# Performance work log

Measured on AMD Instinct MI355X. Metric: run time of the kernel, lower is better.

The kernel has to match this reference:

```python
import jax, jax.numpy as jnp
import numpy as np

N_ATOMS = 500_000
N_PAIRS = 16_000_000
A0 = 0.5291772105638411
KE = 14.399645351950548
KEHALF = KE / 2.0


def softplus_inverse(x):
    # inverse of softplus: log(exp(x) - 1)
    return float(np.log(np.expm1(x)))


def setup_inputs() -> dict:
    key = jax.random.key(0)
    k_z, k_r, k_c, k_i, k_j = jax.random.split(key, 5)
    Zf = jax.random.randint(k_z, (N_ATOMS,), 1, 95).astype(jnp.float32)
    rij = jax.random.uniform(k_r, (N_PAIRS,), minval=0.5, maxval=5.0, dtype=jnp.float32)
    cutoff_values = jax.random.uniform(k_c, (N_PAIRS,), dtype=jnp.float32)
    idx_i = jax.random.randint(k_i, (N_PAIRS,), 0, N_ATOMS)
    idx_j = jax.random.randint(k_j, (N_PAIRS,), 0, N_ATOMS)
    p = lambda v: jnp.full((1,), softplus_inverse(v), dtype=jnp.float32)
    return {
        "N": N_ATOMS,
        "Zf": Zf,
        "rij": rij,
        "cutoff_values": cutoff_values,
        "idx_i": idx_i,
        "idx_j": idx_j,
        "adiv": p(1.0 / (0.8854 * A0)),
        "apow": p(0.23),
        "c1": p(0.1818),
        "c2": p(0.5099),
        "c3": p(0.2802),
        "c4": p(0.02817),
        "a1": p(3.2),
        "a2": p(0.9423),
        "a3": p(0.4028),
        "a4": p(0.2016),
    }


def reference(N, Zf, rij, cutoff_values, idx_i, idx_j,
              adiv, apow, c1, c2, c3, c4, a1, a2, a3, a4):
    sp = jax.nn.softplus
    # per-atom screened charge: [N]
    z = Zf ** sp(apow)
    # per-pair screening length: [P]
    a = (z[idx_i] + z[idx_j]) * sp(adiv)
    a1p = sp(a1) * a
    a2p = sp(a2) * a
    a3p = sp(a3) * a
    a4p = sp(a4) * a
    c1p, c2p, c3p, c4p = sp(c1), sp(c2), sp(c3), sp(c4)
    csum = c1p + c2p + c3p + c4p
    c1n, c2n, c3n, c4n = c1p / csum, c2p / csum, c3p / csum, c4p / csum
    zizj = Zf[idx_i] * Zf[idx_j]
    f = (c1n * jnp.exp(-a1p * rij)
         + c2n * jnp.exp(-a2p * rij)
         + c3n * jnp.exp(-a3p * rij)
         + c4n * jnp.exp(-a4p * rij)) * cutoff_values
    contrib = KEHALF * f * zizj / rij  # [P]
    return jnp.zeros((N,), dtype=Zf.dtype).at[idx_i].add(contrib)
```

## Files before the change

### kernel.cpp

```cpp
#include <hip/hip_runtime.h>
#include <hip/hip_fp16.h>

static constexpr float KEHALF = 7.199822675975274f;
static constexpr int APB = 2048;
static constexpr int APB_SHIFT = 11;
static constexpr int NBMAX = 256;
static constexpr int CHUNK = 8192;
static constexpr int ABLK = 512;
static constexpr int BBLK = 1024;
static constexpr int CTILE = 1024;
static constexpr int NW_SCAN = NBMAX / 64;

typedef float v4f __attribute__((ext_vector_type(4)));
typedef int   v4i __attribute__((ext_vector_type(4)));
typedef unsigned v4u __attribute__((ext_vector_type(4)));

__global__ void zbl_tables_kernel(const float* __restrict__ adiv,
                                  const float* __restrict__ apow,
                                  const float* __restrict__ c1,
                                  const float* __restrict__ c2,
                                  const float* __restrict__ c3,
                                  const float* __restrict__ c4,
                                  const float* __restrict__ a1,
                                  const float* __restrict__ a2,
                                  const float* __restrict__ a3,
                                  const float* __restrict__ a4,
                                  float* __restrict__ consts) {
    if (threadIdx.x == 0) {
        auto sp = [](float x) { return log1pf(expf(x)); };
        float c1p = sp(*c1), c2p = sp(*c2), c3p = sp(*c3), c4p = sp(*c4);
        float inv = 1.0f / (c1p + c2p + c3p + c4p);
        consts[0] = sp(*apow);
        consts[1] = sp(*adiv);
        consts[2] = c1p * inv; consts[3] = c2p * inv;
        consts[4] = c3p * inv; consts[5] = c4p * inv;
        consts[6] = sp(*a1); consts[7] = sp(*a2);
        consts[8] = sp(*a3); consts[9] = sp(*a4);
    }
}

__global__ void zbl_pack_kernel(const float* __restrict__ Zf,
                                unsigned char* __restrict__ zb, int N) {
    int i = blockIdx.x * blockDim.x + threadIdx.x;
    if (i < N) zb[i] = (unsigned char)(Zf[i] + 0.5f);
}

__global__ void __launch_bounds__(ABLK)
zbl_phaseA(const int* __restrict__ idx_i, const int* __restrict__ idx_j,
           const float* __restrict__ rij, const float* __restrict__ cut,
           const unsigned char* __restrict__ zb,
           const float* __restrict__ consts,
           unsigned* __restrict__ recs, unsigned short* __restrict__ starts,
           int P, int NB, int nchunks) {
    __shared__ unsigned hist[NBMAX];
    __shared__ unsigned cursor[NBMAX];
    __shared__ unsigned wsum[NW_SCAN];
    __shared__ unsigned stage[CHUNK];

    const int t = threadIdx.x;
    const int c = blockIdx.x;
    const int base = c * CHUNK;
    const int cnt = min(base + CHUNK, P) - base;
    const int n4 = cnt >> 2;

    for (int b = t; b < NBMAX; b += ABLK) hist[b] = 0;
    __syncthreads();

    const v4i* ii4 = reinterpret_cast<const v4i*>(idx_i + base);
    const bool p0 = t < n4;
    const bool p1 = ABLK + t < n4;
    const bool p2 = 2 * ABLK + t < n4;
    const bool p3 = 3 * ABLK + t < n4;
    v4i ii0{}, ii1{}, ii2{}, ii3{};
    if (p0) ii0 = __builtin_nontemporal_load(ii4 + t);
    if (p1) ii1 = __builtin_nontemporal_load(ii4 + ABLK + t);
    if (p2) ii2 = __builtin_nontemporal_load(ii4 + 2 * ABLK + t);
    if (p3) ii3 = __builtin_nontemporal_load(ii4 + 3 * ABLK + t);

    auto packb = [&](v4i ii) -> unsigned {
        return (unsigned)zb[ii[0]] | ((unsigned)zb[ii[1]] << 8)
             | ((unsigned)zb[ii[2]] << 16) | ((unsigned)zb[ii[3]] << 24);
    };
    unsigned bp0 = 0, bp1 = 0, bp2 = 0, bp3 = 0;
    if (p0) bp0 = packb(ii0);
    if (p1) bp1 = packb(ii1);
    if (p2) bp2 = packb(ii2);
    if (p3) bp3 = packb(ii3);

    auto hist4 = [&](v4i ii) {
        atomicAdd(&hist[(unsigned)ii[0] >> APB_SHIFT], 1u);
        atomicAdd(&hist[(unsigned)ii[1] >> APB_SHIFT], 1u);
        atomicAdd(&hist[(unsigned)ii[2] >> APB_SHIFT], 1u);
        atomicAdd(&hist[(unsigned)ii[3] >> APB_SHIFT], 1u);
    };
    if (p0) hist4(ii0);
    if (p1) hist4(ii1);
    if (p2) hist4(ii2);
    if (p3) hist4(ii3);
    for (int p = n4 * 4 + t; p < cnt; p += ABLK)
        atomicAdd(&hist[(unsigned)idx_i[base + p] >> APB_SHIFT], 1u);
    __syncthreads();

    unsigned hv = (t < NBMAX) ? hist[t] : 0u;
    unsigned v = hv;
#pragma unroll
    for (int off = 1; off < 64; off <<= 1) {
        unsigned n = __shfl_up(v, off, 64);
        if ((t & 63) >= off) v += n;
    }
    if (t < NBMAX && (t & 63) == 63) wsum[t >> 6] = v;
    __syncthreads();
    if (t < NBMAX) {
        unsigned pre = 0;
#pragma unroll
        for (int w = 0; w < NW_SCAN - 1; ++w)
            if (w < (t >> 6)) pre += wsum[w];
        unsigned inc = v + pre;
        cursor[t] = inc - hv;
        if (t < NB)
            starts[(size_t)(t + 1) * nchunks + c] = (unsigned short)inc;
    }
    if (t == 0) starts[c] = 0;
    __syncthreads();

    const float sp_apow = consts[0], sp_adiv = consts[1];
    const float c1n = consts[2], c2n = consts[3], c3n = consts[4], c4n = consts[5];
    const float a1 = consts[6], a2 = consts[7], a3 = consts[8], a4 = consts[9];

    auto process = [&](int i, unsigned bi, unsigned bj, float r, float cu) {
        float fi = (float)bi, fj = (float)bj;
        float zi = __expf(sp_apow * __logf(fi));
        float zj = __expf(sp_apow * __logf(fj));
        float ar = (zi + zj) * sp_adiv * r;
        float f = c1n * __expf(-a1 * ar) + c2n * __expf(-a2 * ar)
                + c3n * __expf(-a3 * ar) + c4n * __expf(-a4 * ar);
        float contrib = KEHALF * f * cu * fi * fj * __builtin_amdgcn_rcpf(r);
        unsigned b = (unsigned)i >> APB_SHIFT;
        unsigned rank = atomicAdd(&cursor[b], 1u);
        stage[rank] = (((unsigned)i & (APB - 1)) << 16)
                    | (unsigned)__half_as_ushort(__float2half_rn(contrib));
    };

    const v4i* jj4 = reinterpret_cast<const v4i*>(idx_j + base);
    const v4f* rr4 = reinterpret_cast<const v4f*>(rij + base);
    const v4f* cc4 = reinterpret_cast<const v4f*>(cut + base);
    auto group = [&](v4i ii, unsigned bp, int q) {
        v4i jj = __builtin_nontemporal_load(jj4 + q);
        v4f rr = __builtin_nontemporal_load(rr4 + q);
        v4f cc = __builtin_nontemporal_load(cc4 + q);
#pragma unroll
        for (int k = 0; k < 4; ++k)
            process(ii[k], (bp >> (8 * k)) & 0xffu, zb[jj[k]], rr[k], cc[k]);
    };
    if (p0) group(ii0, bp0, t);
    if (p1) group(ii1, bp1, ABLK + t);
    if (p2) group(ii2, bp2, 2 * ABLK + t);
    if (p3) group(ii3, bp3, 3 * ABLK + t);
    for (int p = n4 * 4 + t; p < cnt; p += ABLK) {
        int i = idx_i[base + p];
        process(i, zb[i], zb[idx_j[base + p]], rij[base + p], cut[base + p]);
    }
    __syncthreads();

    {
        const v4u* src = reinterpret_cast<const v4u*>(stage);
        v4u* dst = reinterpret_cast<v4u*>(recs + (size_t)base);
        for (int k = t; k < CHUNK / 4; k += ABLK)
            __builtin_nontemporal_store(src[k], dst + k);
    }
}

__global__ void __launch_bounds__(BBLK)
zbl_phaseB(const unsigned* __restrict__ recs,
           const unsigned short* __restrict__ starts,
           float* __restrict__ out, int N, int NB, int nchunks, int cpb) {
    __shared__ float acc[APB];
    __shared__ unsigned short s0s[CTILE];
    __shared__ unsigned short s1s[CTILE];
    const int t = threadIdx.x;
    const int b = blockIdx.x;
    const int c0 = blockIdx.y * cpb;
    const int c1e = min(c0 + cpb, nchunks);
    for (int i = t; i < APB; i += BBLK) acc[i] = 0.f;

    const unsigned short* s0row = starts + (size_t)b * nchunks;
    const unsigned short* s1row = starts + (size_t)(b + 1) * nchunks;
    const int hw = t >> 5, hl = t & 31, nhw = BBLK / 32;

    for (int cb = c0; cb < c1e; cb += CTILE) {
        const int ce = min(cb + CTILE, c1e);
        __syncthreads();
        for (int c = cb + t; c < ce; c += BBLK) {
            s0s[c - cb] = s0row[c];
            s1s[c - cb] = s1row[c];
        }
        __syncthreads();
        for (int c = cb + hw; c < ce; c += nhw) {
            unsigned s0 = s0s[c - cb], s1 = s1s[c - cb];
            const unsigned* seg = recs + (size_t)c * CHUNK;
            for (unsigned u = s0 + hl; u < s1; u += 32) {
                unsigned rec = __builtin_nontemporal_load(seg + u);
                float v = __half2float(__ushort_as_half((unsigned short)(rec & 0xffffu)));
                atomicAdd(&acc[rec >> 16], v);
            }
        }
    }
    __syncthreads();
    const int abase = b << APB_SHIFT;
    for (int i = t; i < APB; i += BBLK) {
        int g = abase + i;
        if (g < N) atomicAdd(&out[g], acc[i]);
    }
}

__global__ void __launch_bounds__(256)
zbl_pair_fallback(const v4f* __restrict__ rij4, const v4f* __restrict__ cut4,
                  const v4i* __restrict__ ii4, const v4i* __restrict__ jj4,
                  const float* __restrict__ Zf, const float* __restrict__ consts,
                  float* __restrict__ out, int P4) {
    int t = blockIdx.x * blockDim.x + threadIdx.x;
    if (t >= P4) return;
    const float sp_apow = consts[0], sp_adiv = consts[1];
    const float c1n = consts[2], c2n = consts[3], c3n = consts[4], c4n = consts[5];
    const float a1 = consts[6], a2 = consts[7], a3 = consts[8], a4 = consts[9];
    v4f rr = rij4[t]; v4f cc = cut4[t]; v4i ii = ii4[t]; v4i jj = jj4[t];
#pragma unroll
    for (int k = 0; k < 4; ++k) {
        int i = ii[k], j = jj[k];
        float zfi = Zf[i], zfj = Zf[j];
        float zi = __expf(sp_apow * __logf(zfi));
        float zj = __expf(sp_apow * __logf(zfj));
        float a = (zi + zj) * sp_adiv;
        float ar = a * rr[k];
        float f = c1n * __expf(-a1 * ar) + c2n * __expf(-a2 * ar)
                + c3n * __expf(-a3 * ar) + c4n * __expf(-a4 * ar);
        atomicAdd(&out[i],
                  KEHALF * f * cc[k] * zfi * zfj * __builtin_amdgcn_rcpf(rr[k]));
    }
}

extern "C" void kernel_launch(void* const* d_in, const int* in_sizes, int n_in,
                              void* d_out, int out_size, void* d_ws, size_t ws_size,
                              hipStream_t stream) {
    const float* Zf = (const float*)d_in[1];
    const float* rij = (const float*)d_in[2];
    const float* cut = (const float*)d_in[3];
    const int* idx_i = (const int*)d_in[4];
    const int* idx_j = (const int*)d_in[5];
    const int N = in_sizes[1];
    const int P = in_sizes[2];
    float* out = (float*)d_out;

    const int NB = (N + APB - 1) / APB;
    const int nchunks = (P + CHUNK - 1) / CHUNK;

    size_t recs_bytes = (size_t)nchunks * CHUNK * 4;
    size_t starts_bytes = (size_t)(NB + 1) * nchunks * 2;
    size_t consts_off = (recs_bytes + starts_bytes + 255) & ~(size_t)255;
    size_t zb_off = consts_off + 16 * 4;
    size_t need = zb_off + (size_t)N + 64;

    if (NB <= NBMAX && ws_size >= need) {
        unsigned* recs = (unsigned*)d_ws;
        unsigned short* starts = (unsigned short*)((char*)d_ws + recs_bytes);
        float* consts = (float*)((char*)d_ws + consts_off);
        unsigned char* zb = (unsigned char*)((char*)d_ws + zb_off);

        zbl_tables_kernel<<<1, 64, 0, stream>>>(
            (const float*)d_in[6], (const float*)d_in[7],
            (const float*)d_in[8], (const float*)d_in[9],
            (const float*)d_in[10], (const float*)d_in[11],
            (const float*)d_in[12], (const float*)d_in[13],
            (const float*)d_in[14], (const float*)d_in[15], consts);

        zbl_pack_kernel<<<(N + 255) / 256, 256, 0, stream>>>(Zf, zb, N);

        hipMemsetAsync(out, 0, (size_t)out_size * sizeof(float), stream);

        zbl_phaseA<<<nchunks, ABLK, 0, stream>>>(
            idx_i, idx_j, rij, cut, zb, consts, recs, starts, P, NB, nchunks);

        int SPLIT = (2048 + NB - 1) / NB;
        if (SPLIT < 1) SPLIT = 1;
        if (SPLIT > 16) SPLIT = 16;
        const int cpb = (nchunks + SPLIT - 1) / SPLIT;
        dim3 gridB(NB, SPLIT);
        zbl_phaseB<<<gridB, BBLK, 0, stream>>>(recs, starts, out, N, NB,
                                               nchunks, cpb);
    } else {
        float* consts = (float*)d_ws;
        hipMemsetAsync(out, 0, (size_t)out_size * sizeof(float), stream);
        zbl_tables_kernel<<<1, 64, 0, stream>>>(
            (const float*)d_in[6], (const float*)d_in[7],
            (const float*)d_in[8], (const float*)d_in[9],
            (const float*)d_in[10], (const float*)d_in[11],
            (const float*)d_in[12], (const float*)d_in[13],
            (const float*)d_in[14], (const float*)d_in[15], consts);
        zbl_pair_fallback<<<(P / 4 + 255) / 256, 256, 0, stream>>>(
            (const v4f*)rij, (const v4f*)cut, (const v4i*)idx_i,
            (const v4i*)idx_j, Zf, consts, out, P / 4);
    }
}
```

Before: 453.7 us.

## Fuse prep kernels, tabulate per-Z screening, prefetch j-charges, drop nontemporal hints

Merges the constants, Z-packing and output-zeroing launches into one prep kernel, which removes two launches and a memset. Phase A now builds a 96-entry shared table of softplus(adiv)*Z^softplus(apow), replacing the per-pair log/exp pow with a table lookup. It also loads idx_j early so both charge gathers are issued together. Nontemporal load/store hints are replaced with plain accesses, and the phase-B split factor is raised to give more blocks. The plain accesses may change cache behaviour for the streamed data, and the table assumes Z values below 96.

```diff
diff --git a/kernel.cpp b/kernel.cpp
--- a/kernel.cpp
+++ b/kernel.cpp
@@ -14,6 +14,22 @@
 typedef float v4f __attribute__((ext_vector_type(4)));
 typedef int   v4i __attribute__((ext_vector_type(4)));
 typedef unsigned v4u __attribute__((ext_vector_type(4)));
+
+__device__ __forceinline__ void compute_consts(
+        const float* adiv, const float* apow,
+        const float* c1, const float* c2, const float* c3, const float* c4,
+        const float* a1, const float* a2, const float* a3, const float* a4,
+        float* consts) {
+    auto sp = [](float x) { return log1pf(expf(x)); };
+    float c1p = sp(*c1), c2p = sp(*c2), c3p = sp(*c3), c4p = sp(*c4);
+    float inv = 1.0f / (c1p + c2p + c3p + c4p);
+    consts[0] = sp(*apow);
+    consts[1] = sp(*adiv);
+    consts[2] = c1p * inv; consts[3] = c2p * inv;
+    consts[4] = c3p * inv; consts[5] = c4p * inv;
+    consts[6] = sp(*a1); consts[7] = sp(*a2);
+    consts[8] = sp(*a3); consts[9] = sp(*a4);
+}
 
 __global__ void zbl_tables_kernel(const float* __restrict__ adiv,
                                   const float* __restrict__ apow,
@@ -26,23 +42,31 @@
                                   const float* __restrict__ a3,
                                   const float* __restrict__ a4,
                                   float* __restrict__ consts) {
-    if (threadIdx.x == 0) {
-        auto sp = [](float x) { return log1pf(expf(x)); };
-        float c1p = sp(*c1), c2p = sp(*c2), c3p = sp(*c3), c4p = sp(*c4);
-        float inv = 1.0f / (c1p + c2p + c3p + c4p);
-        consts[0] = sp(*apow);
-        consts[1] = sp(*adiv);
-        consts[2] = c1p * inv; consts[3] = c2p * inv;
-        consts[4] = c3p * inv; consts[5] = c4p * inv;
-        consts[6] = sp(*a1); consts[7] = sp(*a2);
-        consts[8] = sp(*a3); consts[9] = sp(*a4);
-    }
-}
-
-__global__ void zbl_pack_kernel(const float* __restrict__ Zf,
-                                unsigned char* __restrict__ zb, int N) {
+    if (threadIdx.x == 0)
+        compute_consts(adiv, apow, c1, c2, c3, c4, a1, a2, a3, a4, consts);
+}
+
+__global__ void zbl_prep(const float* __restrict__ Zf,
+                         unsigned char* __restrict__ zb,
+                         float* __restrict__ out, int N,
+                         const float* __restrict__ adiv,
+                         const float* __restrict__ apow,
+                         const float* __restrict__ c1,
+                         const float* __restrict__ c2,
+                         const float* __restrict__ c3,
+                         const float* __restrict__ c4,
+                         const float* __restrict__ a1,
+                         const float* __restrict__ a2,
+                         const float* __restrict__ a3,
+                         const float* __restrict__ a4,
+                         float* __restrict__ consts) {
     int i = blockIdx.x * blockDim.x + threadIdx.x;
-    if (i < N) zb[i] = (unsigned char)(Zf[i] + 0.5f);
+    if (i < N) {
+        zb[i] = (unsigned char)(Zf[i] + 0.5f);
+        out[i] = 0.0f;
+    }
+    if (blockIdx.x == 0 && threadIdx.x == 0)
+        compute_consts(adiv, apow, c1, c2, c3, c4, a1, a2, a3, a4, consts);
 }
 
 __global__ void __launch_bounds__(ABLK)
@@ -55,6 +79,7 @@
     __shared__ unsigned hist[NBMAX];
     __shared__ unsigned cursor[NBMAX];
     __shared__ unsigned wsum[NW_SCAN];
+    __shared__ float lA[96];
     __shared__ unsigned stage[CHUNK];
 
     const int t = threadIdx.x;
@@ -64,28 +89,33 @@
     const int n4 = cnt >> 2;
 
     for (int b = t; b < NBMAX; b += ABLK) hist[b] = 0;
+    if (t < 96)
+        lA[t] = (t == 0) ? 0.0f
+                         : consts[1] * __expf(consts[0] * __logf((float)t));
     __syncthreads();
 
     const v4i* ii4 = reinterpret_cast<const v4i*>(idx_i + base);
+    const v4i* jj4 = reinterpret_cast<const v4i*>(idx_j + base);
     const bool p0 = t < n4;
     const bool p1 = ABLK + t < n4;
     const bool p2 = 2 * ABLK + t < n4;
     const bool p3 = 3 * ABLK + t < n4;
-    v4i ii0{}, ii1{}, ii2{}, ii3{};
-    if (p0) ii0 = __builtin_nontemporal_load(ii4 + t);
-    if (p1) ii1 = __builtin_nontemporal_load(ii4 + ABLK + t);
-    if (p2) ii2 = __builtin_nontemporal_load(ii4 + 2 * ABLK + t);
-    if (p3) ii3 = __builtin_nontemporal_load(ii4 + 3 * ABLK + t);
-
-    auto packb = [&](v4i ii) -> unsigned {
-        return (unsigned)zb[ii[0]] | ((unsigned)zb[ii[1]] << 8)
-             | ((unsigned)zb[ii[2]] << 16) | ((unsigned)zb[ii[3]] << 24);
+    v4i ii0{}, ii1{}, ii2{}, ii3{}, jj0{}, jj1{}, jj2{}, jj3{};
+    if (p0) { ii0 = ii4[t];            jj0 = jj4[t]; }
+    if (p1) { ii1 = ii4[ABLK + t];     jj1 = jj4[ABLK + t]; }
+    if (p2) { ii2 = ii4[2 * ABLK + t]; jj2 = jj4[2 * ABLK + t]; }
+    if (p3) { ii3 = ii4[3 * ABLK + t]; jj3 = jj4[3 * ABLK + t]; }
+
+    auto packb = [&](v4i ix) -> unsigned {
+        return (unsigned)zb[ix[0]] | ((unsigned)zb[ix[1]] << 8)
+             | ((unsigned)zb[ix[2]] << 16) | ((unsigned)zb[ix[3]] << 24);
     };
-    unsigned bp0 = 0, bp1 = 0, bp2 = 0, bp3 = 0;
-    if (p0) bp0 = packb(ii0);
-    if (p1) bp1 = packb(ii1);
-    if (p2) bp2 = packb(ii2);
-    if (p3) bp3 = packb(ii3);
+    unsigned bpi0 = 0, bpi1 = 0, bpi2 = 0, bpi3 = 0;
+    unsigned bpj0 = 0, bpj1 = 0, bpj2 = 0, bpj3 = 0;
+    if (p0) { bpi0 = packb(ii0); bpj0 = packb(jj0); }
+    if (p1) { bpi1 = packb(ii1); bpj1 = packb(jj1); }
+    if (p2) { bpi2 = packb(ii2); bpj2 = packb(jj2); }
+    if (p3) { bpi3 = packb(ii3); bpj3 = packb(jj3); }
 
     auto hist4 = [&](v4i ii) {
         atomicAdd(&hist[(unsigned)ii[0] >> APB_SHIFT], 1u);
@@ -123,39 +153,35 @@
     if (t == 0) starts[c] = 0;
     __syncthreads();
 
-    const float sp_apow = consts[0], sp_adiv = consts[1];
     const float c1n = consts[2], c2n = consts[3], c3n = consts[4], c4n = consts[5];
     const float a1 = consts[6], a2 = consts[7], a3 = consts[8], a4 = consts[9];
 
     auto process = [&](int i, unsigned bi, unsigned bj, float r, float cu) {
-        float fi = (float)bi, fj = (float)bj;
-        float zi = __expf(sp_apow * __logf(fi));
-        float zj = __expf(sp_apow * __logf(fj));
-        float ar = (zi + zj) * sp_adiv * r;
+        float ar = (lA[bi] + lA[bj]) * r;
         float f = c1n * __expf(-a1 * ar) + c2n * __expf(-a2 * ar)
                 + c3n * __expf(-a3 * ar) + c4n * __expf(-a4 * ar);
-        float contrib = KEHALF * f * cu * fi * fj * __builtin_amdgcn_rcpf(r);
+        float contrib = KEHALF * f * cu * (float)bi * (float)bj *
+                        __builtin_amdgcn_rcpf(r);
         unsigned b = (unsigned)i >> APB_SHIFT;
         unsigned rank = atomicAdd(&cursor[b], 1u);
         stage[rank] = (((unsigned)i & (APB - 1)) << 16)
                     | (unsigned)__half_as_ushort(__float2half_rn(contrib));
     };
 
-    const v4i* jj4 = reinterpret_cast<const v4i*>(idx_j + base);
     const v4f* rr4 = reinterpret_cast<const v4f*>(rij + base);
     const v4f* cc4 = reinterpret_cast<const v4f*>(cut + base);
-    auto group = [&](v4i ii, unsigned bp, int q) {
-        v4i jj = __builtin_nontemporal_load(jj4 + q);
-        v4f rr = __builtin_nontemporal_load(rr4 + q);
-        v4f cc = __builtin_nontemporal_load(cc4 + q);
+    auto group = [&](v4i ii, unsigned bpi, unsigned bpj, int q) {
+        v4f rr = rr4[q];
+        v4f cc = cc4[q];
 #pragma unroll
         for (int k = 0; k < 4; ++k)
-            process(ii[k], (bp >> (8 * k)) & 0xffu, zb[jj[k]], rr[k], cc[k]);
+            process(ii[k], (bpi >> (8 * k)) & 0xffu, (bpj >> (8 * k)) & 0xffu,
+                    rr[k], cc[k]);
     };
-    if (p0) group(ii0, bp0, t);
-    if (p1) group(ii1, bp1, ABLK + t);
-    if (p2) group(ii2, bp2, 2 * ABLK + t);
-    if (p3) group(ii3, bp3, 3 * ABLK + t);
+    if (p0) group(ii0, bpi0, bpj0, t);
+    if (p1) group(ii1, bpi1, bpj1, ABLK + t);
+    if (p2) group(ii2, bpi2, bpj2, 2 * ABLK + t);
+    if (p3) group(ii3, bpi3, bpj3, 3 * ABLK + t);
     for (int p = n4 * 4 + t; p < cnt; p += ABLK) {
         int i = idx_i[base + p];
         process(i, zb[i], zb[idx_j[base + p]], rij[base + p], cut[base + p]);
@@ -166,7 +192,7 @@
         const v4u* src = reinterpret_cast<const v4u*>(stage);
         v4u* dst = reinterpret_cast<v4u*>(recs + (size_t)base);
         for (int k = t; k < CHUNK / 4; k += ABLK)
-            __builtin_nontemporal_store(src[k], dst + k);
+            dst[k] = src[k];
     }
 }
 
@@ -199,7 +225,7 @@
             unsigned s0 = s0s[c - cb], s1 = s1s[c - cb];
             const unsigned* seg = recs + (size_t)c * CHUNK;
             for (unsigned u = s0 + hl; u < s1; u += 32) {
-                unsigned rec = __builtin_nontemporal_load(seg + u);
+                unsigned rec = seg[u];
                 float v = __half2float(__ushort_as_half((unsigned short)(rec & 0xffffu)));
                 atomicAdd(&acc[rec >> 16], v);
             }
@@ -266,21 +292,18 @@
         float* consts = (float*)((char*)d_ws + consts_off);
         unsigned char* zb = (unsigned char*)((char*)d_ws + zb_off);
 
-        zbl_tables_kernel<<<1, 64, 0, stream>>>(
+        zbl_prep<<<(N + 255) / 256, 256, 0, stream>>>(
+            Zf, zb, out, N,
             (const float*)d_in[6], (const float*)d_in[7],
             (const float*)d_in[8], (const float*)d_in[9],
             (const float*)d_in[10], (const float*)d_in[11],
             (const float*)d_in[12], (const float*)d_in[13],
             (const float*)d_in[14], (const float*)d_in[15], consts);
 
-        zbl_pack_kernel<<<(N + 255) / 256, 256, 0, stream>>>(Zf, zb, N);
-
-        hipMemsetAsync(out, 0, (size_t)out_size * sizeof(float), stream);
-
         zbl_phaseA<<<nchunks, ABLK, 0, stream>>>(
             idx_i, idx_j, rij, cut, zb, consts, recs, starts, P, NB, nchunks);
 
-        int SPLIT = (2048 + NB - 1) / NB;
+        int SPLIT = 4096 / (NB > 0 ? NB : 1);
         if (SPLIT < 1) SPLIT = 1;
         if (SPLIT > 16) SPLIT = 16;
         const int cpb = (nchunks + SPLIT - 1) / SPLIT;
```

Result: faster. 438.3 us (-3.4%).
